# Kernel optimization log

Measured on AMD Instinct MI355X. Metric: run time of the kernel, lower is better.

## Reference

```python
import jax, jax.numpy as jnp
import numpy as np

CONF = 0.3      # confidence threshold (NMS.conf)
IOU = 0.6       # IoU threshold (NMS.iou)
MAX_WH = 4096.0 # class-offset trick for per-class NMS
K = 2048        # max candidates entering NMS (yolov5-style cap)
MAX_DET = 300   # max detections kept per image (fixed output size)


def setup_inputs() -> dict:
    key = jax.random.key(0)
    kxy, kwh, kobj, kcls = jax.random.split(key, 4)
    B, N, NC = 8, 25200, 80
    # realistic raw predictions: xywh in pixel units for a 640x640 image
    xy = jax.random.uniform(kxy, (B, N, 2), minval=0.0, maxval=640.0)
    wh = jax.random.uniform(kwh, (B, N, 2), minval=2.0, maxval=160.0)
    obj = jax.random.uniform(kobj, (B, N, 1))
    cls = jax.random.uniform(kcls, (B, N, NC))
    x = jnp.concatenate([xy, wh, obj, cls], axis=-1)  # [B, N, 5+NC]
    return {"x": x}


def _xywh2xyxy(b):
    xy, half = b[..., :2], b[..., 2:4] * 0.5
    return jnp.concatenate([xy - half, xy + half], axis=-1)


def _pairwise_iou(boxes):  # boxes: [K, 4] xyxy -> [K, K]
    lt = jnp.maximum(boxes[:, None, :2], boxes[None, :, :2])
    rb = jnp.minimum(boxes[:, None, 2:], boxes[None, :, 2:])
    inter = jnp.clip(rb - lt, 0.0).prod(-1)
    area = (boxes[:, 2] - boxes[:, 0]) * (boxes[:, 3] - boxes[:, 1])
    return inter / (area[:, None] + area[None, :] - inter + 1e-9)


def _nms_single(pred):  # pred: [N, 5+NC]
    obj = pred[:, 4]
    cls_conf = pred[:, 5:] * obj[:, None]          # conf = obj * cls prob
    conf = cls_conf.max(-1)
    cls_id = jnp.argmax(cls_conf, -1)
    valid = (obj > CONF) & (conf > CONF)           # candidate + final threshold
    boxes = _xywh2xyxy(pred[:, :4])
    scores = jnp.where(valid, conf, -1.0)
    top_s, idx = jax.lax.top_k(scores, K)          # cap candidates, sorted desc
    boxes_k = boxes[idx]
    cls_k = cls_id[idx]
    valid_k = top_s > 0.0
    # offset boxes by class so NMS is per-class
    shifted = boxes_k + cls_k[:, None].astype(boxes_k.dtype) * MAX_WH
    iou = _pairwise_iou(shifted)                   # [K, K]
    order = jnp.arange(K)

    def body(keep, i):  # greedy suppression in score order
        active = keep[i] & valid_k[i]
        sup = (iou[i] > IOU) & (order > i)
        keep = jnp.where(active, keep & ~sup, keep)
        return keep, None

    keep, _ = jax.lax.scan(body, jnp.ones((K,), bool), order)
    keep = keep & valid_k
    final_s = jnp.where(keep, top_s, -1.0)
    det_s, det_i = jax.lax.top_k(final_s, MAX_DET)
    dets = jnp.concatenate(
        [boxes_k[det_i], top_s[det_i][:, None],
         cls_k[det_i][:, None].astype(boxes_k.dtype)], axis=-1)  # [MAX_DET, 6]
    return dets, det_s > 0.0


def reference(x):
    # returns (dets [B, MAX_DET, 6] = xyxy,conf,cls ; valid mask [B, MAX_DET])
    return jax.vmap(_nms_single)(x)
```

## Files before the change

### kernel.cpp

```cpp
#include <hip/hip_runtime.h>
#include <hip/hip_bf16.h>

#define B 8
#define N 25200
#define ROW 85
#define NC 80
#define K 2048
#define MAXDET 300
#define NBUCKET 16384
#define CAND_CAP 4096
#define NCHUNK 32
#define STILE 64

__global__ void __launch_bounds__(256)
nms_score_kernel(const float* __restrict__ x,
                 float* __restrict__ scores,
                 int* __restrict__ cls_id) {
    int b = blockIdx.y;
    int i0 = blockIdx.x * STILE;
    int rows = N - i0; if (rows > STILE) rows = STILE;
    __shared__ float lx[STILE * ROW];
    {
        const float4* s4 = (const float4*)(x + ((size_t)b * N + i0) * ROW);
        float4* d4 = (float4*)lx;
        int nv = rows * ROW / 4;
        for (int k = threadIdx.x; k < nv; k += 256) d4[k] = s4[k];
    }
    __syncthreads();
    int g = threadIdx.x >> 2;
    int q = threadIdx.x & 3;
    if (g >= rows) return;
    const float* p = lx + g * ROW;
    float obj = p[4];
    float best = -1e30f;
    int bc = 127;
    if (obj > 0.3f) {
        #pragma unroll
        for (int k = 0; k < 20; ++k) {
            int c = q + 4 * k;
            float v = __fmul_rn(p[5 + c], obj);
            if (v > best) { best = v; bc = c; }
        }
    }
    #pragma unroll
    for (int m = 1; m < 4; m <<= 1) {
        float ov = __shfl_xor(best, m, 64);
        int   oc = __shfl_xor(bc, m, 64);
        if (ov > best || (ov == best && oc < bc)) { best = ov; bc = oc; }
    }
    if (q == 0) {
        int i = i0 + g;
        float score = (obj > 0.3f && best > 0.3f) ? best : -1.0f;
        scores[b * N + i] = score;
        cls_id[b * N + i] = (bc == 127) ? 0 : bc;
    }
}

__global__ void __launch_bounds__(1024, 1)
nms_select_kernel(const float* __restrict__ scores,
                  const float* __restrict__ x,
                  const int* __restrict__ cls_id,
                  float* __restrict__ top_s,
                  float* __restrict__ boxes,
                  int* __restrict__ clsk,
                  float* __restrict__ shifted,
                  float* __restrict__ area) {
    __shared__ unsigned loff[NBUCKET];
    __shared__ unsigned lcnt16[NBUCKET / 2];
    __shared__ unsigned long long lk[CAND_CAP];
    __shared__ unsigned wsum[16];

    int b = blockIdx.x;
    int t = threadIdx.x;
    int ln = t & 63, wv = t >> 6;
    constexpr int NITER = (N + 1023) / 1024;

    {
        uint4 z = {0u, 0u, 0u, 0u};
        uint4* d1 = (uint4*)loff;
        for (int k = t; k < NBUCKET / 4; k += 1024) d1[k] = z;
        uint4* d2 = (uint4*)lcnt16;
        for (int k = t; k < NBUCKET / 8; k += 1024) d2[k] = z;
    }
    for (int k = t; k < CAND_CAP; k += 1024) lk[k] = 0ULL;
    __syncthreads();

    float sreg[NITER];
    #pragma unroll
    for (int r = 0; r < NITER; ++r) {
        int i = t + r * 1024;
        float s = (i < N) ? scores[b * N + i] : -1.0f;
        sreg[r] = s;
        if (s > 0.0f) {
            int q = (int)(__fmul_rn(s, 16384.0f));
            if (q > NBUCKET - 1) q = NBUCKET - 1;
            atomicAdd(&loff[q], 1u);
        }
    }
    __syncthreads();

    unsigned v[16];
    int base_j = t * 16;
    unsigned A4 = (unsigned)(NBUCKET - 16 - base_j) / 4;
    {
        uint4 u0 = ((uint4*)loff)[A4 + 0];
        uint4 u1 = ((uint4*)loff)[A4 + 1];
        uint4 u2 = ((uint4*)loff)[A4 + 2];
        uint4 u3 = ((uint4*)loff)[A4 + 3];
        unsigned u[16] = {u0.x,u0.y,u0.z,u0.w, u1.x,u1.y,u1.z,u1.w,
                          u2.x,u2.y,u2.z,u2.w, u3.x,u3.y,u3.z,u3.w};
        #pragma unroll
        for (int k = 0; k < 16; ++k) v[k] = u[15 - k];
    }
    unsigned S = 0;
    #pragma unroll
    for (int k = 0; k < 16; ++k) S += v[k];
    unsigned pref = S;
    #pragma unroll
    for (int o = 1; o < 64; o <<= 1) { unsigned u = __shfl_up(pref, o, 64); if (ln >= o) pref += u; }
    if (ln == 63) wsum[wv] = pref;
    __syncthreads();
    unsigned wbase = 0;
    for (int w = 0; w < wv; ++w) wbase += wsum[w];
    unsigned running = wbase + pref - S;
    {
        unsigned o[16];
        #pragma unroll
        for (int k = 0; k < 16; ++k) { o[15 - k] = running; running += v[k]; }
        ((uint4*)loff)[A4 + 0] = make_uint4(o[0],  o[1],  o[2],  o[3]);
        ((uint4*)loff)[A4 + 1] = make_uint4(o[4],  o[5],  o[6],  o[7]);
        ((uint4*)loff)[A4 + 2] = make_uint4(o[8],  o[9],  o[10], o[11]);
        ((uint4*)loff)[A4 + 3] = make_uint4(o[12], o[13], o[14], o[15]);
    }
    __syncthreads();

    #pragma unroll
    for (int r = 0; r < NITER; ++r) {
        float s = sreg[r];
        if (s > 0.0f) {
            int i = t + r * 1024;
            int q = (int)(__fmul_rn(s, 16384.0f));
            if (q > NBUCKET - 1) q = NBUCKET - 1;
            unsigned start = loff[q];
            if (start < CAND_CAP) {
                unsigned sh = (q & 1) * 16;
                unsigned old = atomicAdd(&lcnt16[q >> 1], 1u << sh);
                unsigned rank = (old >> sh) & 0xFFFFu;
                unsigned pos = start + rank;
                if (pos < CAND_CAP) {
                    unsigned long long key =
                        ((unsigned long long)__float_as_uint(s) << 32) | (unsigned)(~i);
                    lk[pos] = key;
                }
            }
        }
    }
    __syncthreads();

    for (int q = t; q < NBUCKET; q += 1024) {
        unsigned start = loff[q];
        if (start < CAND_CAP) {
            unsigned c = (lcnt16[q >> 1] >> ((q & 1) * 16)) & 0xFFFFu;
            unsigned m = c;
            if (m > CAND_CAP - start) m = CAND_CAP - start;
            if (m >= 2) {
                for (unsigned a = start + 1; a < start + m; ++a) {
                    unsigned long long kv = lk[a];
                    unsigned p2 = a;
                    while (p2 > start && lk[p2 - 1] < kv) { lk[p2] = lk[p2 - 1]; --p2; }
                    lk[p2] = kv;
                }
            }
        }
    }
    __syncthreads();

    for (int r = t; r < K; r += 1024) {
        unsigned long long key = lk[r];
        float s;
        int idx;
        float x1, y1, x2, y2;
        int c;
        if (key == 0ULL) {
            s = -1.0f; x1 = y1 = x2 = y2 = 0.0f; c = 0;
        } else {
            s = __uint_as_float((unsigned)(key >> 32));
            idx = (int)(~(unsigned)key);
            const float* p = x + ((size_t)b * N + idx) * ROW;
            float cx = p[0], cy = p[1], w = p[2], h = p[3];
            float hx = __fmul_rn(w, 0.5f);
            float hy = __fmul_rn(h, 0.5f);
            x1 = __fsub_rn(cx, hx); y1 = __fsub_rn(cy, hy);
            x2 = __fadd_rn(cx, hx); y2 = __fadd_rn(cy, hy);
            c = cls_id[b * N + idx];
        }
        int o = b * K + r;
        top_s[o] = s;
        boxes[o * 4 + 0] = x1; boxes[o * 4 + 1] = y1;
        boxes[o * 4 + 2] = x2; boxes[o * 4 + 3] = y2;
        clsk[o] = c;
        float sh = __fmul_rn((float)c, 4096.0f);
        float sx1 = __fadd_rn(x1, sh), sy1 = __fadd_rn(y1, sh);
        float sx2 = __fadd_rn(x2, sh), sy2 = __fadd_rn(y2, sh);
        shifted[o * 4 + 0] = sx1; shifted[o * 4 + 1] = sy1;
        shifted[o * 4 + 2] = sx2; shifted[o * 4 + 3] = sy2;
        area[o] = __fmul_rn(__fsub_rn(sx2, sx1), __fsub_rn(sy2, sy1));
    }
}

__global__ void nms_mask_kernel(const float* __restrict__ shifted,
                                const float* __restrict__ area,
                                unsigned long long* __restrict__ maskT,
                                unsigned long long* __restrict__ nzT) {
    int L = blockIdx.x, b = blockIdx.y;
    int jb = (int)((__fsqrt_rn(8.0f * (float)L + 1.0f) - 1.0f) * 0.5f);
    while ((jb + 1) * (jb + 2) / 2 <= L) ++jb;
    while (jb * (jb + 1) / 2 > L) --jb;
    int ib = L - jb * (jb + 1) / 2;
    int t = threadIdx.x;
    int i = ib * 64 + t;

    __shared__ float jbox[64][4];
    __shared__ float jarea[64];
    int j0 = jb * 64;
    {
        const float* sb = shifted + ((size_t)b * K + j0 + t) * 4;
        jbox[t][0] = sb[0]; jbox[t][1] = sb[1]; jbox[t][2] = sb[2]; jbox[t][3] = sb[3];
        jarea[t] = area[b * K + j0 + t];
    }
    __syncthreads();

    const float* ab = shifted + ((size_t)b * K + i) * 4;
    float ax1 = ab[0], ay1 = ab[1], ax2 = ab[2], ay2 = ab[3];
    float aarea = area[b * K + i];

    unsigned long long mycol = 0ULL;
    for (int jl = 0; jl < 64; ++jl) {
        int j = j0 + jl;
        bool cond = false;
        if (j > i) {
            float lx = fmaxf(ax1, jbox[jl][0]);
            float ly = fmaxf(ay1, jbox[jl][1]);
            float rx = fminf(ax2, jbox[jl][2]);
            float ry = fminf(ay2, jbox[jl][3]);
            float w = fmaxf(__fsub_rn(rx, lx), 0.0f);
            float h = fmaxf(__fsub_rn(ry, ly), 0.0f);
            float inter = __fmul_rn(w, h);
            float denom = __fadd_rn(__fsub_rn(__fadd_rn(aarea, jarea[jl]), inter), 1e-9f);
            float iou = __fdiv_rn(inter, denom);
            cond = iou > 0.6f;
        }
        unsigned long long colm = __ballot(cond);
        if (t == jl) mycol = colm;
    }
    maskT[((size_t)b * K + j0 + t) * NCHUNK + ib] = mycol;
    unsigned long long nzb = __ballot(mycol != 0ULL);
    if (t == 0) nzT[((size_t)b * NCHUNK + jb) * NCHUNK + ib] = nzb;
}

__global__ void __launch_bounds__(1024)
nms_reduce_out_kernel(const unsigned long long* __restrict__ maskT,
                      const unsigned long long* __restrict__ nzT,
                      const float* __restrict__ top_s,
                      const float* __restrict__ boxes,
                      const int* __restrict__ clsk,
                      float* __restrict__ out) {
    int b = blockIdx.x;
    int t = threadIdx.x;
    int ln = t & 63, wv = t >> 6;
    __shared__ unsigned long long kept[NCHUNK], decided[NCHUNK];
    __shared__ unsigned long long snapk[NCHUNK], snapd[NCHUNK];
    __shared__ int nundec;
    if (t == 0) nundec = 0;
    __syncthreads();

    int st[2];
    #pragma unroll
    for (int h = 0; h < 2; ++h) {
        int c = wv + h * 16;
        int j = c * 64 + ln;
        unsigned long long w = (ln < NCHUNK)
            ? nzT[((size_t)b * NCHUNK + c) * NCHUNK + ln] : 0ULL;
        #pragma unroll
        for (int m = 1; m < 64; m <<= 1) w |= __shfl_xor(w, m, 64);
        bool valid = top_s[b * K + j] > 0.0f;
        bool hassup = ((w >> ln) & 1ULL) != 0ULL;
        bool k_local = valid && !hassup;
        bool d_local = !valid || !hassup;
        st[h] = d_local ? 1 : 0;
        unsigned long long kb = __ballot(k_local);
        unsigned long long db = __ballot(d_local);
        if (ln == 0) {
            kept[c] = kb;
            decided[c] = db;
            if (~db != 0ULL) atomicAdd(&nundec, __popcll(~db));
        }
    }

    for (int round = 0; round < 2048; ++round) {
        __syncthreads();
        if (nundec == 0) break;
        if (t < NCHUNK) { snapd[t] = decided[t]; snapk[t] = kept[t]; }
        __syncthreads();
        #pragma unroll
        for (int h = 0; h < 2; ++h) {
            if (st[h]) continue;
            int j = t + h * 1024;
            const unsigned long long* row = maskT + ((size_t)b * K + j) * NCHUNK;
            int nw = (j >> 6) + 1;
            unsigned long long pend = 0ULL, sup = 0ULL;
            for (int w = 0; w < nw; ++w) {
                unsigned long long r = row[w];
                pend |= r & ~snapd[w];
                sup  |= r & snapk[w];
            }
            if (pend == 0ULL) {
                unsigned long long bit = 1ULL << (j & 63);
                if (sup == 0ULL) atomicOr(&kept[j >> 6], bit);
                atomicOr(&decided[j >> 6], bit);
                st[h] = 1;
                atomicSub(&nundec, 1);
            }
        }
    }
    __syncthreads();

    if (wv == 0) {
        int lane = ln;
        int total = 0;
        for (int c = 0; c < NCHUNK; ++c) {
            bool k = ((kept[c] >> lane) & 1ULL) != 0ULL;
            unsigned long long m = __ballot(k);
            total += __popcll(m);
        }
        float* dets  = out + (size_t)b * MAXDET * 6;
        float* flags = out + (size_t)B * MAXDET * 6 + (size_t)b * MAXDET;
        unsigned long long below = (lane == 0) ? 0ULL : (~0ULL >> (64 - lane));
        int kc = 0, nc = 0;
        for (int c = 0; c < NCHUNK; ++c) {
            int i = c * 64 + lane;
            bool k = ((kept[c] >> lane) & 1ULL) != 0ULL;
            unsigned long long m = __ballot(k);
            int pc = __popcll(m);
            int slot = k ? (kc + __popcll(m & below))
                         : (total + nc + __popcll((~m) & below));
            if (slot < MAXDET) {
                int o = b * K + i;
                dets[slot * 6 + 0] = boxes[o * 4 + 0];
                dets[slot * 6 + 1] = boxes[o * 4 + 1];
                dets[slot * 6 + 2] = boxes[o * 4 + 2];
                dets[slot * 6 + 3] = boxes[o * 4 + 3];
                dets[slot * 6 + 4] = top_s[o];
                dets[slot * 6 + 5] = (float)clsk[o];
                flags[slot] = k ? 1.0f : 0.0f;
            }
            kc += pc;
            nc += 64 - pc;
        }
    }
}

extern "C" void kernel_launch(void* const* d_in, const int* in_sizes, int n_in,
                              void* d_out, int out_size, void* d_ws, size_t ws_size,
                              hipStream_t stream) {
    const float* x = (const float*)d_in[0];
    float* out = (float*)d_out;

    char* ws = (char*)d_ws;
    size_t off = 0;
    auto alloc = [&](size_t bytes) -> void* {
        void* p = ws + off;
        off += bytes;
        off = (off + 255) & ~(size_t)255;
        return p;
    };

    float*    scores = (float*)    alloc((size_t)B * N * 4);
    int*      cls_id = (int*)      alloc((size_t)B * N * 4);
    float*    top_s  = (float*)    alloc((size_t)B * K * 4);
    float*    boxes  = (float*)    alloc((size_t)B * K * 4 * 4);
    int*      clsk   = (int*)      alloc((size_t)B * K * 4);
    float*    shifted= (float*)    alloc((size_t)B * K * 4 * 4);
    float*    area   = (float*)    alloc((size_t)B * K * 4);
    unsigned long long* maskT = (unsigned long long*) alloc((size_t)B * K * NCHUNK * 8);
    unsigned long long* nzT   = (unsigned long long*) alloc((size_t)B * NCHUNK * NCHUNK * 8);
    (void)ws_size;

    nms_score_kernel<<<dim3((N + STILE - 1) / STILE, B), 256, 0, stream>>>(x, scores, cls_id);
    nms_select_kernel<<<B, 1024, 0, stream>>>(scores, x, cls_id,
                                              top_s, boxes, clsk, shifted, area);
    nms_mask_kernel<<<dim3(NCHUNK * (NCHUNK + 1) / 2, B), 64, 0, stream>>>(shifted, area, maskT, nzT);
    nms_reduce_out_kernel<<<B, 1024, 0, stream>>>(maskT, nzT, top_s, boxes, clsk, out);
}
```

Before: 160.9 us.

## Replace full IoU mask and parallel reduction with per-class greedy NMS blocks

Drops the triangular K×K suppression-mask kernel and the iterative fixed-point reduction. Instead, one 64-thread block per (class, image) gathers that class's valid candidates in score order and runs greedy suppression with wavefront ballots, setting global keep bits atomically. This relies on the class-offset trick meaning boxes of different classes never overlap, so cross-class IoU work is skipped. A small output kernel then compacts the kept detections. The cost is a sequential loop over each class's candidates and atomics on global keep bits.

```diff
diff --git a/kernel.cpp b/kernel.cpp
--- a/kernel.cpp
+++ b/kernel.cpp
@@ -64,7 +64,8 @@
                   float* __restrict__ boxes,
                   int* __restrict__ clsk,
                   float* __restrict__ shifted,
-                  float* __restrict__ area) {
+                  float* __restrict__ area,
+                  unsigned long long* __restrict__ keepbits) {
     __shared__ unsigned loff[NBUCKET];
     __shared__ unsigned lcnt16[NBUCKET / 2];
     __shared__ unsigned long long lk[CAND_CAP];
@@ -74,6 +75,8 @@
     int t = threadIdx.x;
     int ln = t & 63, wv = t >> 6;
     constexpr int NITER = (N + 1023) / 1024;
+
+    if (t < NCHUNK) keepbits[b * NCHUNK + t] = 0ULL;
 
     {
         uint4 z = {0u, 0u, 0u, 0u};
@@ -208,155 +211,145 @@
     }
 }
 
-__global__ void nms_mask_kernel(const float* __restrict__ shifted,
-                                const float* __restrict__ area,
-                                unsigned long long* __restrict__ maskT,
-                                unsigned long long* __restrict__ nzT) {
-    int L = blockIdx.x, b = blockIdx.y;
-    int jb = (int)((__fsqrt_rn(8.0f * (float)L + 1.0f) - 1.0f) * 0.5f);
-    while ((jb + 1) * (jb + 2) / 2 <= L) ++jb;
-    while (jb * (jb + 1) / 2 > L) --jb;
-    int ib = L - jb * (jb + 1) / 2;
+__global__ void __launch_bounds__(64)
+nms_class_kernel(const float* __restrict__ top_s,
+                 const int* __restrict__ clsk,
+                 const float* __restrict__ shifted,
+                 const float* __restrict__ area,
+                 unsigned long long* __restrict__ keepbits) {
+    int c = blockIdx.x, b = blockIdx.y;
     int t = threadIdx.x;
-    int i = ib * 64 + t;
-
-    __shared__ float jbox[64][4];
-    __shared__ float jarea[64];
-    int j0 = jb * 64;
-    {
-        const float* sb = shifted + ((size_t)b * K + j0 + t) * 4;
-        jbox[t][0] = sb[0]; jbox[t][1] = sb[1]; jbox[t][2] = sb[2]; jbox[t][3] = sb[3];
-        jarea[t] = area[b * K + j0 + t];
-    }
-    __syncthreads();
-
-    const float* ab = shifted + ((size_t)b * K + i) * 4;
-    float ax1 = ab[0], ay1 = ab[1], ax2 = ab[2], ay2 = ab[3];
-    float aarea = area[b * K + i];
-
-    unsigned long long mycol = 0ULL;
-    for (int jl = 0; jl < 64; ++jl) {
-        int j = j0 + jl;
-        bool cond = false;
-        if (j > i) {
-            float lx = fmaxf(ax1, jbox[jl][0]);
-            float ly = fmaxf(ay1, jbox[jl][1]);
-            float rx = fminf(ax2, jbox[jl][2]);
-            float ry = fminf(ay2, jbox[jl][3]);
-            float w = fmaxf(__fsub_rn(rx, lx), 0.0f);
-            float h = fmaxf(__fsub_rn(ry, ly), 0.0f);
-            float inter = __fmul_rn(w, h);
-            float denom = __fadd_rn(__fsub_rn(__fadd_rn(aarea, jarea[jl]), inter), 1e-9f);
-            float iou = __fdiv_rn(inter, denom);
-            cond = iou > 0.6f;
-        }
-        unsigned long long colm = __ballot(cond);
-        if (t == jl) mycol = colm;
-    }
-    maskT[((size_t)b * K + j0 + t) * NCHUNK + ib] = mycol;
-    unsigned long long nzb = __ballot(mycol != 0ULL);
-    if (t == 0) nzT[((size_t)b * NCHUNK + jb) * NCHUNK + ib] = nzb;
-}
-
-__global__ void __launch_bounds__(1024)
-nms_reduce_out_kernel(const unsigned long long* __restrict__ maskT,
-                      const unsigned long long* __restrict__ nzT,
-                      const float* __restrict__ top_s,
-                      const float* __restrict__ boxes,
-                      const int* __restrict__ clsk,
-                      float* __restrict__ out) {
+    unsigned long long below = (t == 0) ? 0ULL : (~0ULL >> (64 - t));
+
+    __shared__ int srank[K];
+    __shared__ unsigned long long skeep[NCHUNK];
+
+    int n = 0;
+    for (int ch = 0; ch < NCHUNK; ++ch) {
+        int r = ch * 64 + t;
+        bool sel = (clsk[b * K + r] == c) && (top_s[b * K + r] > 0.0f);
+        unsigned long long m = __ballot(sel);
+        if (sel) srank[n + __popcll(m & below)] = r;
+        n += __popcll(m);
+    }
+    __syncthreads();
+    if (n == 0) return;
+
+    if (n <= 64) {
+        float x1 = 0.f, y1 = 0.f, x2 = 0.f, y2 = 0.f, ar = 0.f;
+        int r = -1;
+        if (t < n) {
+            r = srank[t];
+            const float* sb = shifted + ((size_t)b * K + r) * 4;
+            x1 = sb[0]; y1 = sb[1]; x2 = sb[2]; y2 = sb[3];
+            ar = area[b * K + r];
+        }
+        unsigned long long keepw = (n == 64) ? ~0ULL : ((1ULL << n) - 1ULL);
+        for (int i = 0; i < n; ++i) {
+            if (!((keepw >> i) & 1ULL)) continue;
+            float bx1 = __shfl(x1, i, 64), by1 = __shfl(y1, i, 64);
+            float bx2 = __shfl(x2, i, 64), by2 = __shfl(y2, i, 64);
+            float ba  = __shfl(ar, i, 64);
+            bool cond = false;
+            if (t > i && t < n) {
+                float lx = fmaxf(bx1, x1), ly = fmaxf(by1, y1);
+                float rx = fminf(bx2, x2), ry = fminf(by2, y2);
+                float w = fmaxf(__fsub_rn(rx, lx), 0.0f);
+                float h = fmaxf(__fsub_rn(ry, ly), 0.0f);
+                float inter = __fmul_rn(w, h);
+                float denom = __fadd_rn(__fsub_rn(__fadd_rn(ba, ar), inter), 1e-9f);
+                cond = __fdiv_rn(inter, denom) > 0.6f;
+            }
+            keepw &= ~__ballot(cond);
+        }
+        if (t < n && ((keepw >> t) & 1ULL))
+            atomicOr(&keepbits[b * NCHUNK + (r >> 6)], 1ULL << (r & 63));
+        return;
+    }
+
+    for (int w = t; w < NCHUNK; w += 64) {
+        int lo = w * 64;
+        unsigned long long vw;
+        if (n >= lo + 64)      vw = ~0ULL;
+        else if (n <= lo)      vw = 0ULL;
+        else                   vw = (1ULL << (n - lo)) - 1ULL;
+        skeep[w] = vw;
+    }
+    __syncthreads();
+    for (int i = 0; i < n; ++i) {
+        if (!((skeep[i >> 6] >> (i & 63)) & 1ULL)) continue;
+        int ri = srank[i];
+        const float* sbi = shifted + ((size_t)b * K + ri) * 4;
+        float bx1 = sbi[0], by1 = sbi[1], bx2 = sbi[2], by2 = sbi[3];
+        float ba = area[b * K + ri];
+        int jb_hi = (n - 1) >> 6;
+        for (int jb2 = (i + 1) >> 6; jb2 <= jb_hi; ++jb2) {
+            int j = jb2 * 64 + t;
+            bool cond = false;
+            if (j > i && j < n) {
+                int rj = srank[j];
+                const float* sbj = shifted + ((size_t)b * K + rj) * 4;
+                float x1 = sbj[0], y1 = sbj[1], x2 = sbj[2], y2 = sbj[3];
+                float arj = area[b * K + rj];
+                float lx = fmaxf(bx1, x1), ly = fmaxf(by1, y1);
+                float rx = fminf(bx2, x2), ry = fminf(by2, y2);
+                float w = fmaxf(__fsub_rn(rx, lx), 0.0f);
+                float h = fmaxf(__fsub_rn(ry, ly), 0.0f);
+                float inter = __fmul_rn(w, h);
+                float denom = __fadd_rn(__fsub_rn(__fadd_rn(ba, arj), inter), 1e-9f);
+                cond = __fdiv_rn(inter, denom) > 0.6f;
+            }
+            unsigned long long sup = __ballot(cond);
+            if (t == 0) skeep[jb2] &= ~sup;
+        }
+        __syncthreads();
+    }
+    for (int j = t; j < n; j += 64) {
+        if ((skeep[j >> 6] >> (j & 63)) & 1ULL) {
+            int r = srank[j];
+            atomicOr(&keepbits[b * NCHUNK + (r >> 6)], 1ULL << (r & 63));
+        }
+    }
+}
+
+__global__ void __launch_bounds__(64)
+nms_out_kernel(const unsigned long long* __restrict__ keepbits,
+               const float* __restrict__ top_s,
+               const float* __restrict__ boxes,
+               const int* __restrict__ clsk,
+               float* __restrict__ out) {
     int b = blockIdx.x;
-    int t = threadIdx.x;
-    int ln = t & 63, wv = t >> 6;
-    __shared__ unsigned long long kept[NCHUNK], decided[NCHUNK];
-    __shared__ unsigned long long snapk[NCHUNK], snapd[NCHUNK];
-    __shared__ int nundec;
-    if (t == 0) nundec = 0;
-    __syncthreads();
-
-    int st[2];
-    #pragma unroll
-    for (int h = 0; h < 2; ++h) {
-        int c = wv + h * 16;
-        int j = c * 64 + ln;
-        unsigned long long w = (ln < NCHUNK)
-            ? nzT[((size_t)b * NCHUNK + c) * NCHUNK + ln] : 0ULL;
-        #pragma unroll
-        for (int m = 1; m < 64; m <<= 1) w |= __shfl_xor(w, m, 64);
-        bool valid = top_s[b * K + j] > 0.0f;
-        bool hassup = ((w >> ln) & 1ULL) != 0ULL;
-        bool k_local = valid && !hassup;
-        bool d_local = !valid || !hassup;
-        st[h] = d_local ? 1 : 0;
-        unsigned long long kb = __ballot(k_local);
-        unsigned long long db = __ballot(d_local);
-        if (ln == 0) {
-            kept[c] = kb;
-            decided[c] = db;
-            if (~db != 0ULL) atomicAdd(&nundec, __popcll(~db));
-        }
-    }
-
-    for (int round = 0; round < 2048; ++round) {
-        __syncthreads();
-        if (nundec == 0) break;
-        if (t < NCHUNK) { snapd[t] = decided[t]; snapk[t] = kept[t]; }
-        __syncthreads();
-        #pragma unroll
-        for (int h = 0; h < 2; ++h) {
-            if (st[h]) continue;
-            int j = t + h * 1024;
-            const unsigned long long* row = maskT + ((size_t)b * K + j) * NCHUNK;
-            int nw = (j >> 6) + 1;
-            unsigned long long pend = 0ULL, sup = 0ULL;
-            for (int w = 0; w < nw; ++w) {
-                unsigned long long r = row[w];
-                pend |= r & ~snapd[w];
-                sup  |= r & snapk[w];
-            }
-            if (pend == 0ULL) {
-                unsigned long long bit = 1ULL << (j & 63);
-                if (sup == 0ULL) atomicOr(&kept[j >> 6], bit);
-                atomicOr(&decided[j >> 6], bit);
-                st[h] = 1;
-                atomicSub(&nundec, 1);
-            }
-        }
-    }
-    __syncthreads();
-
-    if (wv == 0) {
-        int lane = ln;
-        int total = 0;
-        for (int c = 0; c < NCHUNK; ++c) {
-            bool k = ((kept[c] >> lane) & 1ULL) != 0ULL;
-            unsigned long long m = __ballot(k);
-            total += __popcll(m);
-        }
-        float* dets  = out + (size_t)b * MAXDET * 6;
-        float* flags = out + (size_t)B * MAXDET * 6 + (size_t)b * MAXDET;
-        unsigned long long below = (lane == 0) ? 0ULL : (~0ULL >> (64 - lane));
-        int kc = 0, nc = 0;
-        for (int c = 0; c < NCHUNK; ++c) {
-            int i = c * 64 + lane;
-            bool k = ((kept[c] >> lane) & 1ULL) != 0ULL;
-            unsigned long long m = __ballot(k);
-            int pc = __popcll(m);
-            int slot = k ? (kc + __popcll(m & below))
-                         : (total + nc + __popcll((~m) & below));
-            if (slot < MAXDET) {
-                int o = b * K + i;
-                dets[slot * 6 + 0] = boxes[o * 4 + 0];
-                dets[slot * 6 + 1] = boxes[o * 4 + 1];
-                dets[slot * 6 + 2] = boxes[o * 4 + 2];
-                dets[slot * 6 + 3] = boxes[o * 4 + 3];
-                dets[slot * 6 + 4] = top_s[o];
-                dets[slot * 6 + 5] = (float)clsk[o];
-                flags[slot] = k ? 1.0f : 0.0f;
-            }
-            kc += pc;
-            nc += 64 - pc;
-        }
+    int lane = threadIdx.x;
+    __shared__ unsigned long long kept[NCHUNK];
+    if (lane < NCHUNK) kept[lane] = keepbits[b * NCHUNK + lane];
+    __syncthreads();
+
+    int total = 0;
+    for (int c = 0; c < NCHUNK; ++c) total += __popcll(kept[c]);
+
+    float* dets  = out + (size_t)b * MAXDET * 6;
+    float* flags = out + (size_t)B * MAXDET * 6 + (size_t)b * MAXDET;
+    unsigned long long below = (lane == 0) ? 0ULL : (~0ULL >> (64 - lane));
+    int kc = 0, nc2 = 0;
+    for (int c = 0; c < NCHUNK; ++c) {
+        int i = c * 64 + lane;
+        unsigned long long m = kept[c];
+        bool k = ((m >> lane) & 1ULL) != 0ULL;
+        int pc = __popcll(m);
+        int slot = k ? (kc + __popcll(m & below))
+                     : (total + nc2 + __popcll((~m) & below));
+        if (slot < MAXDET) {
+            int o = b * K + i;
+            dets[slot * 6 + 0] = boxes[o * 4 + 0];
+            dets[slot * 6 + 1] = boxes[o * 4 + 1];
+            dets[slot * 6 + 2] = boxes[o * 4 + 2];
+            dets[slot * 6 + 3] = boxes[o * 4 + 3];
+            dets[slot * 6 + 4] = top_s[o];
+            dets[slot * 6 + 5] = (float)clsk[o];
+            flags[slot] = k ? 1.0f : 0.0f;
+        }
+        kc += pc;
+        nc2 += 64 - pc;
     }
 }
 
@@ -382,13 +375,12 @@
     int*      clsk   = (int*)      alloc((size_t)B * K * 4);
     float*    shifted= (float*)    alloc((size_t)B * K * 4 * 4);
     float*    area   = (float*)    alloc((size_t)B * K * 4);
-    unsigned long long* maskT = (unsigned long long*) alloc((size_t)B * K * NCHUNK * 8);
-    unsigned long long* nzT   = (unsigned long long*) alloc((size_t)B * NCHUNK * NCHUNK * 8);
+    unsigned long long* keepbits = (unsigned long long*) alloc((size_t)B * NCHUNK * 8);
     (void)ws_size;
 
     nms_score_kernel<<<dim3((N + STILE - 1) / STILE, B), 256, 0, stream>>>(x, scores, cls_id);
     nms_select_kernel<<<B, 1024, 0, stream>>>(scores, x, cls_id,
-                                              top_s, boxes, clsk, shifted, area);
-    nms_mask_kernel<<<dim3(NCHUNK * (NCHUNK + 1) / 2, B), 64, 0, stream>>>(shifted, area, maskT, nzT);
-    nms_reduce_out_kernel<<<B, 1024, 0, stream>>>(maskT, nzT, top_s, boxes, clsk, out);
-}
+                                              top_s, boxes, clsk, shifted, area, keepbits);
+    nms_class_kernel<<<dim3(NC, B), 64, 0, stream>>>(top_s, clsk, shifted, area, keepbits);
+    nms_out_kernel<<<B, 64, 0, stream>>>(keepbits, top_s, boxes, clsk, out);
+}
```

After: 145.4 us. 9.6% less time.
